# Optimization experiments

Hardware: AMD Instinct MI355X
Metric: run time of the kernel (lower is better)

## Reference

```python
import jax, jax.numpy as jnp
import numpy as np

BN_EPS = 1e-5


def _conv_bn_relu(x, w, gamma, beta):
    # 3x3 conv, stride 1, pad 1, no bias, NCHW; BatchNorm in training mode (batch stats)
    y = jax.lax.conv_general_dilated(x, w, (1, 1), ((1, 1), (1, 1)),
                                     dimension_numbers=('NCHW', 'OIHW', 'NCHW'))
    mu = y.mean(axis=(0, 2, 3), keepdims=True)
    var = y.var(axis=(0, 2, 3), keepdims=True)  # biased var, as torch BN uses for normalization
    y = (y - mu) * jax.lax.rsqrt(var + BN_EPS)
    y = y * gamma[None, :, None, None] + beta[None, :, None, None]
    return jax.nn.relu(y)


def setup_inputs() -> dict:
    key = jax.random.key(0)
    ks = jax.random.split(key, 12)
    N, C, h, w, H, W = 64, 256, 8, 8, 32, 32
    OC, NC = 256, 80
    inp = {
        'z_f': jax.random.normal(ks[0], (N, C, h, w), jnp.float32),
        'x_f': jax.random.normal(ks[1], (N, C, H, W), jnp.float32),
        'conv_cls_w': 0.05 * jax.random.normal(ks[2], (OC, C + 1, 3, 3), jnp.float32),
        'bn_cls_g': jnp.ones((OC,), jnp.float32),
        'bn_cls_b': jnp.zeros((OC,), jnp.float32),
        'conv_reg_w': 0.05 * jax.random.normal(ks[3], (OC, C + 1, 3, 3), jnp.float32),
        'bn_reg_g': jnp.ones((OC,), jnp.float32),
        'bn_reg_b': jnp.zeros((OC,), jnp.float32),
        'lin_cls_w': 0.01 * jax.random.normal(ks[4], (NC, OC * h * w), jnp.float32),
        'lin_cls_b': jnp.zeros((NC,), jnp.float32),
        'lin_reg_w': 0.01 * jax.random.normal(ks[5], (4 * NC, OC * H * W), jnp.float32),
        'lin_reg_b': jnp.zeros((4 * NC,), jnp.float32),
    }
    return inp


def reference(z_f, x_f, conv_cls_w, bn_cls_g, bn_cls_b, conv_reg_w, bn_reg_g, bn_reg_b,
              lin_cls_w, lin_cls_b, lin_reg_w, lin_reg_b):
    N, C, h, w = z_f.shape
    H, W = x_f.shape[2], x_f.shape[3]
    z = z_f.reshape(N, C, h * w)            # (N, C, hw)
    x = x_f.reshape(N, C, H * W)            # (N, C, HW)
    zt = z.transpose(0, 2, 1)               # (N, hw, C)
    xt = x.transpose(0, 2, 1)               # (N, HW, C)
    # batched pairwise squared-distance + sigmoid transform
    # NOTE: the original batched (ndim==3) path does NOT divide by sqrt(C)
    xs = jnp.sum(zt * zt, axis=-1)[:, :, None]          # (N, hw, 1)
    ys = jnp.sum(xt * xt, axis=-1)[:, None, :]          # (N, 1, HW)
    d = xs + ys - 2.0 * jnp.einsum('npc,nqc->npq', zt, xt)  # (N, hw, HW)
    d = 4.0 * jax.nn.sigmoid(-d) - 1.0     # == 4/(1+exp(d)) - 1, numerically stable
    dist_t = d.min(axis=1, keepdims=True)                    # (N, 1, HW)
    dist_s = d.min(axis=2, keepdims=True).transpose(0, 2, 1)  # (N, 1, hw)
    feat_cls = jnp.concatenate([dist_s, z], axis=1).reshape(N, C + 1, h, w)
    feat_loc = jnp.concatenate([dist_t, x], axis=1).reshape(N, C + 1, H, W)
    fc = _conv_bn_relu(feat_cls, conv_cls_w, bn_cls_g, bn_cls_b)   # (N, OC, h, w)
    fl = _conv_bn_relu(feat_loc, conv_reg_w, bn_reg_g, bn_reg_b)   # (N, OC, H, W)
    cls = fc.reshape(N, -1) @ lin_cls_w.T + lin_cls_b              # (N, n_classes)
    loc = fl.reshape(N, -1) @ lin_reg_w.T + lin_reg_b              # (N, 4*n_classes)
    return (cls, loc)
```

## Files before the change

kernel.cpp:

```cpp
#include <hip/hip_runtime.h>
#include <math.h>

typedef short short8 __attribute__((ext_vector_type(8)));
typedef float f32x4 __attribute__((ext_vector_type(4)));
typedef unsigned int uint4v __attribute__((ext_vector_type(4)));

#define WS_DS_ENC 0
#define WS_DT     4096
#define WS_SUMS   69632
#define WS_SS     70656
#define WS_YCLS   71680
#define WS_YREG   595968
#define WS_XT     8984576
#define WS_ZT     17373184
#define WS_WTR    17897472
#define WS_WTDR   18192384
#define WS_WTC    18196480
#define WS_WTDC   18491392
#define WS_PART   18495488
#define WS_XSQ    28981248
#define WS_ZSQ    29046784

__device__ __forceinline__ float dsig(float d) {
    return 4.0f / (1.0f + __expf(d)) - 1.0f;
}
__device__ __forceinline__ unsigned fenc(float f) {
    unsigned u = __float_as_uint(f);
    return (u & 0x80000000u) ? ~u : (u | 0x80000000u);
}
__device__ __forceinline__ float fdec(unsigned e) {
    unsigned u = (e & 0x80000000u) ? (e ^ 0x80000000u) : ~e;
    return __uint_as_float(u);
}
__device__ __forceinline__ unsigned short f2bf(float f) {
    unsigned u = __float_as_uint(f);
    return (unsigned short)((u + 0x7fffu + ((u >> 16) & 1u)) >> 16);
}
__device__ __forceinline__ float bf2f(unsigned short h) {
    return __uint_as_float(((unsigned)h) << 16);
}
__device__ __forceinline__ short8 pack8_trunc(const float* f) {
    uint4v u;
#pragma unroll
    for (int i = 0; i < 4; ++i) {
        unsigned lo = __float_as_uint(f[2 * i]) >> 16;
        unsigned hi = __float_as_uint(f[2 * i + 1]) & 0xffff0000u;
        u[i] = lo | hi;
    }
    return __builtin_bit_cast(short8, u);
}

__global__ void k_init(unsigned* __restrict__ ds_enc, float* __restrict__ sums,
                       float* __restrict__ out_cls, float* __restrict__ out_loc,
                       const float* __restrict__ lin_cls_b, const float* __restrict__ lin_reg_b) {
    int i = blockIdx.x * 256 + threadIdx.x;
    if (i < 4096) ds_enc[i] = 0u;
    if (i < 1024) sums[i] = 0.0f;
    if (i < 5120) out_cls[i] = lin_cls_b[i % 80];
    if (i < 20480) out_loc[i] = lin_reg_b[i % 320];
}

__global__ __launch_bounds__(256) void k_xt(const float* __restrict__ x, unsigned short* __restrict__ xt,
                                            float* __restrict__ xsq) {
    __shared__ float t[64 * 33];
    __shared__ float xr[4][32];
    const int n = blockIdx.x, row = blockIdx.y;
    const int tid = threadIdx.x;
    const int col = tid & 31, g = tid >> 5;
    float sq = 0.f;
    for (int c4 = 0; c4 < 4; ++c4) {
        const int ic0 = c4 * 64;
        __syncthreads();
        {
            int icl = tid >> 2, cg = tid & 3;
            const float* src = &x[((n * 256 + ic0 + icl) * 32 + row) * 32 + cg * 8];
            float4 a = *reinterpret_cast<const float4*>(src);
            float4 b = *reinterpret_cast<const float4*>(src + 4);
            float* d = &t[icl * 33 + cg * 8];
            d[0] = a.x; d[1] = a.y; d[2] = a.z; d[3] = a.w;
            d[4] = b.x; d[5] = b.y; d[6] = b.z; d[7] = b.w;
        }
        __syncthreads();
        {
            short8 v;
#pragma unroll
            for (int j = 0; j < 8; ++j) {
                float f = t[(g * 8 + j) * 33 + col];
                sq = fmaf(f, f, sq);
                v[j] = (short)f2bf(f);
            }
            *reinterpret_cast<short8*>(&xt[((n * 32 + row) * 32 + col) * 256 + ic0 + g * 8]) = v;
        }
    }
    sq += __shfl_xor(sq, 32);
    if ((tid & 63) < 32) xr[tid >> 6][col] = sq;
    __syncthreads();
    if (tid < 32) xsq[(n * 32 + row) * 32 + tid] = xr[0][tid] + xr[1][tid] + xr[2][tid] + xr[3][tid];
}

__global__ __launch_bounds__(256) void k_zt(const float* __restrict__ z, unsigned short* __restrict__ zt,
                                            float* __restrict__ zsq) {
    __shared__ float t[64 * 65];
    __shared__ float zr[4][64];
    const int n = blockIdx.x;
    const int tid = threadIdx.x;
    const int pos = tid & 63, gg = tid >> 6;
    float sq = 0.f;
    for (int c4 = 0; c4 < 4; ++c4) {
        const int ic0 = c4 * 64;
        __syncthreads();
        {
            int icl = tid >> 2, pg = tid & 3;
            const float* src = &z[(n * 256 + ic0 + icl) * 64 + pg * 16];
#pragma unroll
            for (int r = 0; r < 4; ++r) {
                float4 a = *reinterpret_cast<const float4*>(src + r * 4);
                float* d = &t[icl * 65 + pg * 16 + r * 4];
                d[0] = a.x; d[1] = a.y; d[2] = a.z; d[3] = a.w;
            }
        }
        __syncthreads();
        {
            short8 v0, v1;
#pragma unroll
            for (int j = 0; j < 8; ++j) {
                float f = t[(gg * 16 + j) * 65 + pos];
                sq = fmaf(f, f, sq);
                v0[j] = (short)f2bf(f);
            }
#pragma unroll
            for (int j = 0; j < 8; ++j) {
                float f = t[(gg * 16 + 8 + j) * 65 + pos];
                sq = fmaf(f, f, sq);
                v1[j] = (short)f2bf(f);
            }
            unsigned short* d = &zt[(n * 64 + pos) * 256 + ic0 + gg * 16];
            *reinterpret_cast<short8*>(d) = v0;
            *reinterpret_cast<short8*>(d + 8) = v1;
        }
    }
    zr[gg][pos] = sq;
    __syncthreads();
    if (tid < 64) zsq[n * 64 + tid] = zr[0][tid] + zr[1][tid] + zr[2][tid] + zr[3][tid];
}

__global__ void k_wswz(const float* __restrict__ wr, const float* __restrict__ wc,
                       unsigned short* __restrict__ wtr, unsigned short* __restrict__ wtdr,
                       unsigned short* __restrict__ wtc, unsigned short* __restrict__ wtdc) {
    const int idx = blockIdx.x * 256 + threadIdx.x;
    const float* src = blockIdx.y ? wc : wr;
    unsigned short* dw = blockIdx.y ? wtc : wtr;
    unsigned short* dd = blockIdx.y ? wtdc : wtdr;
    if (idx < 73728) {
        int tap = idx >> 13, rem = idx & 8191;
        int kc = rem >> 10, rem2 = rem & 1023;
        int q = rem2 >> 8, oc = rem2 & 255;
        short8 v;
#pragma unroll
        for (int j = 0; j < 8; ++j) {
            int icg = 1 + kc * 32 + q * 8 + j;
            v[j] = (short)f2bf(src[(oc * 257 + icg) * 9 + tap]);
        }
        *reinterpret_cast<short8*>(&dw[idx * 8]) = v;
    } else if (idx < 74752) {
        int i2 = idx - 73728;
        int q = i2 >> 8, oc = i2 & 255;
        short8 v;
#pragma unroll
        for (int j = 0; j < 8; ++j) {
            int k = q * 8 + j;
            v[j] = (k < 9) ? (short)f2bf(src[(oc * 257) * 9 + k]) : (short)0;
        }
        *reinterpret_cast<short8*>(&dd[i2 * 8]) = v;
    }
}

__global__ __launch_bounds__(256) void k_dist(const unsigned short* __restrict__ zt,
                                              const unsigned short* __restrict__ xt,
                                              const float* __restrict__ zsq, const float* __restrict__ xsq,
                                              float* __restrict__ dist_t, unsigned* __restrict__ ds_enc) {
    const int n = blockIdx.y;
    const int tid = threadIdx.x;
    const int wv = tid >> 6, lane = tid & 63;
    const int l15 = lane & 15, q4 = lane >> 4;
    const int q0 = blockIdx.x * 256 + wv * 64;
    const unsigned short* zb = zt + n * 16384;
    const unsigned short* xb = xt + (size_t)(n * 1024 + q0) * 256;

    f32x4 acc[4][4];
#pragma unroll
    for (int mi = 0; mi < 4; ++mi)
#pragma unroll
        for (int ni = 0; ni < 4; ++ni) acc[mi][ni] = (f32x4){0.f, 0.f, 0.f, 0.f};

#pragma unroll
    for (int ks = 0; ks < 8; ++ks) {
        short8 a[4], b[4];
#pragma unroll
        for (int mi = 0; mi < 4; ++mi)
            a[mi] = *reinterpret_cast<const short8*>(&zb[(mi * 16 + l15) * 256 + ks * 32 + q4 * 8]);
#pragma unroll
        for (int ni = 0; ni < 4; ++ni)
            b[ni] = *reinterpret_cast<const short8*>(&xb[(ni * 16 + l15) * 256 + ks * 32 + q4 * 8]);
#pragma unroll
        for (int ni = 0; ni < 4; ++ni)
#pragma unroll
            for (int mi = 0; mi < 4; ++mi)
                acc[mi][ni] = __builtin_amdgcn_mfma_f32_16x16x32_bf16(a[mi], b[ni], acc[mi][ni], 0, 0, 0);
    }

    float zs[4][4];
#pragma unroll
    for (int mi = 0; mi < 4; ++mi)
#pragma unroll
        for (int e = 0; e < 4; ++e) zs[mi][e] = zsq[n * 64 + mi * 16 + q4 * 4 + e];
    float xq[4];
#pragma unroll
    for (int ni = 0; ni < 4; ++ni) xq[ni] = xsq[n * 1024 + q0 + ni * 16 + l15];

#pragma unroll
    for (int ni = 0; ni < 4; ++ni) {
        float m = -1e30f;
#pragma unroll
        for (int mi = 0; mi < 4; ++mi)
#pragma unroll
            for (int e = 0; e < 4; ++e)
                m = fmaxf(m, zs[mi][e] - 2.f * acc[mi][ni][e]);
        m = fmaxf(m, __shfl_xor(m, 16));
        m = fmaxf(m, __shfl_xor(m, 32));
        if (lane < 16) dist_t[n * 1024 + q0 + ni * 16 + l15] = dsig(m + xq[ni]);
    }
#pragma unroll
    for (int mi = 0; mi < 4; ++mi)
#pragma unroll
        for (int e = 0; e < 4; ++e) {
            float v = -1e30f;
#pragma unroll
            for (int ni = 0; ni < 4; ++ni) v = fmaxf(v, xq[ni] - 2.f * acc[mi][ni][e]);
            v = fmaxf(v, __shfl_xor(v, 1));
            v = fmaxf(v, __shfl_xor(v, 2));
            v = fmaxf(v, __shfl_xor(v, 4));
            v = fmaxf(v, __shfl_xor(v, 8));
            if (l15 == 0) atomicMax(&ds_enc[n * 64 + mi * 16 + q4 * 4 + e], fenc(zs[mi][e] + v));
        }
}

__global__ __launch_bounds__(256) void k_conv_reg(
    const unsigned short* __restrict__ xt, const float* __restrict__ dist_t,
    const unsigned short* __restrict__ wt, const unsigned short* __restrict__ wtd,
    unsigned short* __restrict__ y, float* __restrict__ sums) {
    __shared__ __align__(16) char smem[17408];
    unsigned short* As = (unsigned short*)smem;
    unsigned short* Ds = (unsigned short*)(smem + 16320);
    float* Ts = (float*)smem;

    const int n = blockIdx.y;
    const int pt = blockIdx.x >> 1, ot = blockIdx.x & 1;
    const int tid = threadIdx.x;
    const int w = tid >> 6, lane = tid & 63;
    const int l15 = lane & 15, q = lane >> 4;
    const int wm = w & 1, wn = w >> 1;
    const int ocW = ot * 128 + wn * 64;

    f32x4 acc[4][4];
#pragma unroll
    for (int mi = 0; mi < 4; ++mi)
#pragma unroll
        for (int ni = 0; ni < 4; ++ni) acc[mi][ni] = (f32x4){0.f, 0.f, 0.f, 0.f};

    for (int f = tid; f < 204; f += 256) {
        int rr = f / 34, cc = f % 34;
        int prow = pt * 4 + rr;
        float v = 0.f;
        if (prow >= 1 && prow <= 32 && cc >= 1 && cc <= 32)
            v = dist_t[n * 1024 + (prow - 1) * 32 + (cc - 1)];
        Ds[f] = f2bf(v);
    }
    __syncthreads();
    {
        short8 ad[4];
#pragma unroll
        for (int mi = 0; mi < 4; ++mi) {
            int m = wm * 64 + mi * 16 + l15;
            int r = m >> 5, c = m & 31;
            short8 v = {0, 0, 0, 0, 0, 0, 0, 0};
#pragma unroll
            for (int j = 0; j < 8; ++j) {
                int k = q * 8 + j;
                if (k < 9) {
                    int ky = k / 3, kx = k % 3;
                    v[j] = (short)Ds[(r + ky) * 34 + (c + kx)];
                }
            }
            ad[mi] = v;
        }
#pragma unroll
        for (int ni = 0; ni < 4; ++ni) {
            short8 b = *reinterpret_cast<const short8*>(&wtd[(q * 256 + ocW + ni * 16 + l15) * 8]);
#pragma unroll
            for (int mi = 0; mi < 4; ++mi)
                acc[mi][ni] = __builtin_amdgcn_mfma_f32_16x16x32_bf16(ad[mi], b, acc[mi][ni], 0, 0, 0);
        }
    }

    for (int kc = 0; kc < 8; ++kc) {
        __syncthreads();
#pragma unroll
        for (int it = 0; it < 4; ++it) {
            int f = tid + 256 * it;
            if (f < 816) {
                int cell = f >> 2, ch = f & 3;
                int rr = cell / 34, cc = cell % 34;
                int prow = pt * 4 + rr;
                short8 v = {0, 0, 0, 0, 0, 0, 0, 0};
                if (prow >= 1 && prow <= 32 && cc >= 1 && cc <= 32)
                    v = *reinterpret_cast<const short8*>(
                        &xt[((n * 32 + prow - 1) * 32 + cc - 1) * 256 + kc * 32 + ch * 8]);
                *reinterpret_cast<short8*>(&As[cell * 40 + ch * 8]) = v;
            }
        }
        __syncthreads();
#pragma unroll
        for (int tap = 0; tap < 9; ++tap) {
            const int ky = tap / 3, kx = tap % 3;
            short8 a[4];
#pragma unroll
            for (int mi = 0; mi < 4; ++mi) {
                int m = wm * 64 + mi * 16 + l15;
                int r = (m >> 5) + ky, c = (m & 31) + kx;
                a[mi] = *reinterpret_cast<const short8*>(&As[(r * 34 + c) * 40 + q * 8]);
            }
            const unsigned short* wb = wt + (size_t)(((tap * 8 + kc) * 4 + q) * 256) * 8;
#pragma unroll
            for (int ni = 0; ni < 4; ++ni) {
                short8 b = *reinterpret_cast<const short8*>(&wb[(ocW + ni * 16 + l15) * 8]);
#pragma unroll
                for (int mi = 0; mi < 4; ++mi)
                    acc[mi][ni] = __builtin_amdgcn_mfma_f32_16x16x32_bf16(a[mi], b, acc[mi][ni], 0, 0, 0);
            }
        }
    }

#pragma unroll
    for (int ni = 0; ni < 4; ++ni) {
        float s = 0.f, qq = 0.f;
#pragma unroll
        for (int mi = 0; mi < 4; ++mi)
#pragma unroll
            for (int e = 0; e < 4; ++e) {
                float v = acc[mi][ni][e];
                s += v; qq = fmaf(v, v, qq);
            }
        s += __shfl_xor(s, 16); s += __shfl_xor(s, 32);
        qq += __shfl_xor(qq, 16); qq += __shfl_xor(qq, 32);
        if (lane < 16) {
            atomicAdd(&sums[512 + ocW + ni * 16 + l15], s);
            atomicAdd(&sums[768 + ocW + ni * 16 + l15], qq);
        }
    }

    __syncthreads();
    float* T = Ts + w * 1088;
#pragma unroll
    for (int mi = 0; mi < 4; ++mi) {
#pragma unroll
        for (int ni = 0; ni < 4; ++ni)
#pragma unroll
            for (int e = 0; e < 4; ++e)
                T[(ni * 16 + l15) * 17 + q * 4 + e] = acc[mi][ni][e];
#pragma unroll
        for (int eo = 0; eo < 16; ++eo) {
            int ocl = eo * 4 + q;
            float v = T[ocl * 17 + l15];
            y[(size_t)n * 262144 + (size_t)(ocW + ocl) * 1024 + pt * 128 + wm * 64 + mi * 16 + l15] = f2bf(v);
        }
    }
}

__global__ __launch_bounds__(256) void k_conv_cls(
    const unsigned short* __restrict__ zt, const unsigned* __restrict__ ds_enc,
    const unsigned short* __restrict__ wt, const unsigned short* __restrict__ wtd,
    unsigned short* __restrict__ y, float* __restrict__ sums) {
    __shared__ __align__(16) char smem[17408];
    unsigned short* As = (unsigned short*)smem;
    unsigned short* Ds = (unsigned short*)(smem + 16000);
    float* Ts = (float*)smem;

    const int n0 = blockIdx.x * 2;
    const int ob = blockIdx.y;
    const int tid = threadIdx.x;
    const int w = tid >> 6, lane = tid & 63;
    const int l15 = lane & 15, q = lane >> 4;
    const int wm = w & 1, wn = w >> 1;
    const int ocW = ob * 128 + wn * 64;

    f32x4 acc[4][4];
#pragma unroll
    for (int mi = 0; mi < 4; ++mi)
#pragma unroll
        for (int ni = 0; ni < 4; ++ni) acc[mi][ni] = (f32x4){0.f, 0.f, 0.f, 0.f};

    for (int f = tid; f < 200; f += 256) {
        int n_l = f / 100, rem = f % 100;
        int rr = rem / 10, cc = rem % 10;
        float v = 0.f;
        if (rr >= 1 && rr <= 8 && cc >= 1 && cc <= 8)
            v = dsig(fdec(ds_enc[(n0 + n_l) * 64 + (rr - 1) * 8 + (cc - 1)]));
        Ds[f] = f2bf(v);
    }
    __syncthreads();
    {
        short8 ad[4];
#pragma unroll
        for (int mi = 0; mi < 4; ++mi) {
            int pos = mi * 16 + l15;
            int r = pos >> 3, c = pos & 7;
            short8 v = {0, 0, 0, 0, 0, 0, 0, 0};
#pragma unroll
            for (int j = 0; j < 8; ++j) {
                int k = q * 8 + j;
                if (k < 9) {
                    int ky = k / 3, kx = k % 3;
                    v[j] = (short)Ds[wm * 100 + (r + ky) * 10 + (c + kx)];
                }
            }
            ad[mi] = v;
        }
#pragma unroll
        for (int ni = 0; ni < 4; ++ni) {
            short8 b = *reinterpret_cast<const short8*>(&wtd[(q * 256 + ocW + ni * 16 + l15) * 8]);
#pragma unroll
            for (int mi = 0; mi < 4; ++mi)
                acc[mi][ni] = __builtin_amdgcn_mfma_f32_16x16x32_bf16(ad[mi], b, acc[mi][ni], 0, 0, 0);
        }
    }

    for (int kc = 0; kc < 8; ++kc) {
        __syncthreads();
#pragma unroll
        for (int it = 0; it < 4; ++it) {
            int f = tid + 256 * it;
            if (f < 800) {
                int cell = f >> 2, ch = f & 3;
                int n_l = cell / 100, rem = cell % 100;
                int rr = rem / 10, cc = rem % 10;
                short8 v = {0, 0, 0, 0, 0, 0, 0, 0};
                if (rr >= 1 && rr <= 8 && cc >= 1 && cc <= 8)
                    v = *reinterpret_cast<const short8*>(
                        &zt[((n0 + n_l) * 64 + (rr - 1) * 8 + (cc - 1)) * 256 + kc * 32 + ch * 8]);
                *reinterpret_cast<short8*>(&As[cell * 40 + ch * 8]) = v;
            }
        }
        __syncthreads();
#pragma unroll
        for (int tap = 0; tap < 9; ++tap) {
            const int ky = tap / 3, kx = tap % 3;
            short8 a[4];
#pragma unroll
            for (int mi = 0; mi < 4; ++mi) {
                int pos = mi * 16 + l15;
                int r = (pos >> 3) + ky, c = (pos & 7) + kx;
                a[mi] = *reinterpret_cast<const short8*>(&As[(wm * 100 + r * 10 + c) * 40 + q * 8]);
            }
            const unsigned short* wb = wt + (size_t)(((tap * 8 + kc) * 4 + q) * 256) * 8;
#pragma unroll
            for (int ni = 0; ni < 4; ++ni) {
                short8 b = *reinterpret_cast<const short8*>(&wb[(ocW + ni * 16 + l15) * 8]);
#pragma unroll
                for (int mi = 0; mi < 4; ++mi)
                    acc[mi][ni] = __builtin_amdgcn_mfma_f32_16x16x32_bf16(a[mi], b, acc[mi][ni], 0, 0, 0);
            }
        }
    }

#pragma unroll
    for (int ni = 0; ni < 4; ++ni) {
        float s = 0.f, qq = 0.f;
#pragma unroll
        for (int mi = 0; mi < 4; ++mi)
#pragma unroll
            for (int e = 0; e < 4; ++e) {
                float v = acc[mi][ni][e];
                s += v; qq = fmaf(v, v, qq);
            }
        s += __shfl_xor(s, 16); s += __shfl_xor(s, 32);
        qq += __shfl_xor(qq, 16); qq += __shfl_xor(qq, 32);
        if (lane < 16) {
            atomicAdd(&sums[0 + ocW + ni * 16 + l15], s);
            atomicAdd(&sums[256 + ocW + ni * 16 + l15], qq);
        }
    }

    __syncthreads();
    float* T = Ts + w * 1088;
#pragma unroll
    for (int mi = 0; mi < 4; ++mi) {
#pragma unroll
        for (int ni = 0; ni < 4; ++ni)
#pragma unroll
            for (int e = 0; e < 4; ++e)
                T[(ni * 16 + l15) * 17 + q * 4 + e] = acc[mi][ni][e];
#pragma unroll
        for (int eo = 0; eo < 16; ++eo) {
            int ocl = eo * 4 + q;
            float v = T[ocl * 17 + l15];
            y[(size_t)(n0 + wm) * 16384 + (size_t)(ocW + ocl) * 64 + mi * 16 + l15] = f2bf(v);
        }
    }
}

__global__ void k_bnfin(const float* __restrict__ sums,
                        const float* __restrict__ g_cls, const float* __restrict__ b_cls,
                        const float* __restrict__ g_reg, const float* __restrict__ b_reg,
                        float* __restrict__ ss) {
    int t = threadIdx.x;
    {
        float mean = sums[t] * (1.f / 4096.f);
        float var = sums[256 + t] * (1.f / 4096.f) - mean * mean;
        float sc = g_cls[t] * rsqrtf(var + 1e-5f);
        ss[t] = sc;
        ss[256 + t] = b_cls[t] - mean * sc;
    }
    {
        float mean = sums[512 + t] * (1.f / 65536.f);
        float var = sums[768 + t] * (1.f / 65536.f) - mean * mean;
        float sc = g_reg[t] * rsqrtf(var + 1e-5f);
        ss[512 + t] = sc;
        ss[768 + t] = b_reg[t] - mean * sc;
    }
}

__global__ __launch_bounds__(256) void k_lin_cls(const unsigned short* __restrict__ y, const float* __restrict__ ss,
                                                 const float* __restrict__ w, float* __restrict__ out) {
    const int kb = blockIdx.x * 256;
    const int tid = threadIdx.x;
    const int wv = tid >> 6, lane = tid & 63;
    const int l15 = lane & 15, q4 = lane >> 4;
    f32x4 acc[5];
#pragma unroll
    for (int ni = 0; ni < 5; ++ni) acc[ni] = (f32x4){0.f, 0.f, 0.f, 0.f};
#pragma unroll
    for (int ks = 0; ks < 8; ++ks) {
        const int k0 = kb + ks * 32 + q4 * 8;
        short8 yv = *reinterpret_cast<const short8*>(&y[(wv * 16 + l15) * 16384 + k0]);
        const int ch = k0 >> 6;
        const float sc = ss[ch], sh = ss[256 + ch];
        float f[8];
#pragma unroll
        for (int j = 0; j < 8; ++j) f[j] = fmaxf(fmaf(bf2f((unsigned short)yv[j]), sc, sh), 0.f);
        short8 a = pack8_trunc(f);
#pragma unroll
        for (int ni = 0; ni < 5; ++ni) {
            const float* wp = &w[(size_t)(ni * 16 + l15) * 16384 + k0];
            float4 b0 = *reinterpret_cast<const float4*>(wp);
            float4 b1 = *reinterpret_cast<const float4*>(wp + 4);
            float g[8] = {b0.x, b0.y, b0.z, b0.w, b1.x, b1.y, b1.z, b1.w};
            acc[ni] = __builtin_amdgcn_mfma_f32_16x16x32_bf16(a, pack8_trunc(g), acc[ni], 0, 0, 0);
        }
    }
#pragma unroll
    for (int ni = 0; ni < 5; ++ni)
#pragma unroll
        for (int e = 0; e < 4; ++e)
            atomicAdd(&out[(wv * 16 + q4 * 4 + e) * 80 + ni * 16 + l15], acc[ni][e]);
}

__global__ __launch_bounds__(256) void k_lin_reg2(const unsigned short* __restrict__ y, const float* __restrict__ ss,
                                                  const float* __restrict__ w, float* __restrict__ part) {
    __shared__ __align__(16) unsigned short A_l[32 * 520];
    const int k0 = blockIdx.x * 512;
    const int tid = threadIdx.x;
    const int wv = tid >> 6, lane = tid & 63;
    const int l15 = lane & 15, q = lane >> 4;
    const int jw = wv * 80;

    f32x4 acc[5][4];
#pragma unroll
    for (int ni = 0; ni < 5; ++ni)
#pragma unroll
        for (int mi = 0; mi < 4; ++mi) acc[ni][mi] = (f32x4){0.f, 0.f, 0.f, 0.f};

    for (int scn = 0; scn < 2; ++scn) {
        const int ksub = k0 + scn * 256;
        const int ch = ksub >> 10;
        const float scf = ss[512 + ch], shf = ss[768 + ch];
        __syncthreads();
        {
            const int c = tid & 31, nb = tid >> 5;
#pragma unroll
            for (int p = 0; p < 8; ++p) {
                const int n = p * 8 + nb;
                short8 v = *reinterpret_cast<const short8*>(&y[(size_t)n * 262144 + ksub + c * 8]);
                float f[8];
#pragma unroll
                for (int j = 0; j < 8; ++j)
                    f[j] = fmaxf(fmaf(bf2f((unsigned short)v[j]), scf, shf), 0.f);
                *reinterpret_cast<short8*>(&A_l[c * 520 + n * 8]) = pack8_trunc(f);
            }
        }
        __syncthreads();
#pragma unroll
        for (int kk = 0; kk < 8; ++kk) {
            short8 a[4];
#pragma unroll
            for (int mi = 0; mi < 4; ++mi)
                a[mi] = *reinterpret_cast<const short8*>(&A_l[(kk * 4 + q) * 520 + (mi * 16 + l15) * 8]);
            short8 b[5];
#pragma unroll
            for (int ni = 0; ni < 5; ++ni) {
                const float* wp = &w[(size_t)(jw + ni * 16 + l15) * 262144 + ksub + kk * 32 + q * 8];
                float4 b0 = *reinterpret_cast<const float4*>(wp);
                float4 b1 = *reinterpret_cast<const float4*>(wp + 4);
                float f[8] = {b0.x, b0.y, b0.z, b0.w, b1.x, b1.y, b1.z, b1.w};
                b[ni] = pack8_trunc(f);
            }
#pragma unroll
            for (int ni = 0; ni < 5; ++ni)
#pragma unroll
                for (int mi = 0; mi < 4; ++mi)
                    acc[ni][mi] = __builtin_amdgcn_mfma_f32_16x16x32_bf16(a[mi], b[ni], acc[ni][mi], 0, 0, 0);
        }
    }

    float* pb = part + (size_t)blockIdx.x * 20480;
#pragma unroll
    for (int ni = 0; ni < 5; ++ni) {
        const int j = jw + ni * 16 + l15;
#pragma unroll
        for (int mi = 0; mi < 4; ++mi)
#pragma unroll
            for (int e = 0; e < 4; ++e) {
                const int n = mi * 16 + q * 4 + e;
                pb[n * 320 + j] = acc[ni][mi][e];
            }
    }
}

__global__ __launch_bounds__(256) void k_lin_red(const float* __restrict__ part, float* __restrict__ out_loc) {
    const int idx = blockIdx.x * 256 + threadIdx.x;
    const int b0 = blockIdx.y * 128;
    float s0 = 0.f, s1 = 0.f, s2 = 0.f, s3 = 0.f;
#pragma unroll 4
    for (int b = 0; b < 128; b += 4) {
        s0 += part[(size_t)(b0 + b + 0) * 20480 + idx];
        s1 += part[(size_t)(b0 + b + 1) * 20480 + idx];
        s2 += part[(size_t)(b0 + b + 2) * 20480 + idx];
        s3 += part[(size_t)(b0 + b + 3) * 20480 + idx];
    }
    atomicAdd(&out_loc[idx], (s0 + s1) + (s2 + s3));
}

extern "C" void kernel_launch(void* const* d_in, const int* in_sizes, int n_in,
                              void* d_out, int out_size, void* d_ws, size_t ws_size,
                              hipStream_t stream) {
    const float* z_f        = (const float*)d_in[0];
    const float* x_f        = (const float*)d_in[1];
    const float* conv_cls_w = (const float*)d_in[2];
    const float* bn_cls_g   = (const float*)d_in[3];
    const float* bn_cls_b   = (const float*)d_in[4];
    const float* conv_reg_w = (const float*)d_in[5];
    const float* bn_reg_g   = (const float*)d_in[6];
    const float* bn_reg_b   = (const float*)d_in[7];
    const float* lin_cls_w  = (const float*)d_in[8];
    const float* lin_cls_b  = (const float*)d_in[9];
    const float* lin_reg_w  = (const float*)d_in[10];
    const float* lin_reg_b  = (const float*)d_in[11];

    float* out = (float*)d_out;
    float* ws  = (float*)d_ws;
    unsigned* ds_enc = (unsigned*)(ws + WS_DS_ENC);
    float* dist_t = ws + WS_DT;
    float* sums   = ws + WS_SUMS;
    float* ss     = ws + WS_SS;
    unsigned short* y_cls = (unsigned short*)(ws + WS_YCLS);
    unsigned short* y_reg = (unsigned short*)(ws + WS_YREG);
    unsigned short* xt    = (unsigned short*)(ws + WS_XT);
    unsigned short* zt    = (unsigned short*)(ws + WS_ZT);
    unsigned short* wtr   = (unsigned short*)(ws + WS_WTR);
    unsigned short* wtdr  = (unsigned short*)(ws + WS_WTDR);
    unsigned short* wtc   = (unsigned short*)(ws + WS_WTC);
    unsigned short* wtdc  = (unsigned short*)(ws + WS_WTDC);
    float* part   = ws + WS_PART;
    float* xsq    = ws + WS_XSQ;
    float* zsq    = ws + WS_ZSQ;

    hipLaunchKernelGGL(k_init, dim3(80), dim3(256), 0, stream, ds_enc, sums, out, out + 5120, lin_cls_b, lin_reg_b);
    hipLaunchKernelGGL(k_xt, dim3(64, 32), dim3(256), 0, stream, x_f, xt, xsq);
    hipLaunchKernelGGL(k_zt, dim3(64), dim3(256), 0, stream, z_f, zt, zsq);
    hipLaunchKernelGGL(k_wswz, dim3(292, 2), dim3(256), 0, stream, conv_reg_w, conv_cls_w, wtr, wtdr, wtc, wtdc);
    hipLaunchKernelGGL(k_dist, dim3(4, 64), dim3(256), 0, stream, zt, xt, zsq, xsq, dist_t, ds_enc);
    hipLaunchKernelGGL(k_conv_reg, dim3(16, 64), dim3(256), 0, stream, xt, dist_t, wtr, wtdr, y_reg, sums);
    hipLaunchKernelGGL(k_conv_cls, dim3(32, 2), dim3(256), 0, stream, zt, ds_enc, wtc, wtdc, y_cls, sums);
    hipLaunchKernelGGL(k_bnfin, dim3(1), dim3(256), 0, stream, sums, bn_cls_g, bn_cls_b, bn_reg_g, bn_reg_b, ss);
    hipLaunchKernelGGL(k_lin_cls, dim3(64), dim3(256), 0, stream, y_cls, ss, lin_cls_w, out);
    hipLaunchKernelGGL(k_lin_reg2, dim3(512), dim3(256), 0, stream, y_reg, ss, lin_reg_w, part);
    hipLaunchKernelGGL(k_lin_red, dim3(80, 4), dim3(256), 0, stream, part, out + 5120);
}
```

Before: 791.7 us.

## Merge prep, conv, and linear kernels into fewer launches with double-buffered conv staging

New measurement: 761.5 us. -3.8%, faster.

```diff
diff --git a/kernel.cpp b/kernel.cpp
--- a/kernel.cpp
+++ b/kernel.cpp
@@ -49,129 +49,136 @@
     }
     return __builtin_bit_cast(short8, u);
 }
-
-__global__ void k_init(unsigned* __restrict__ ds_enc, float* __restrict__ sums,
-                       float* __restrict__ out_cls, float* __restrict__ out_loc,
-                       const float* __restrict__ lin_cls_b, const float* __restrict__ lin_reg_b) {
-    int i = blockIdx.x * 256 + threadIdx.x;
-    if (i < 4096) ds_enc[i] = 0u;
-    if (i < 1024) sums[i] = 0.0f;
-    if (i < 5120) out_cls[i] = lin_cls_b[i % 80];
-    if (i < 20480) out_loc[i] = lin_reg_b[i % 320];
-}
-
-__global__ __launch_bounds__(256) void k_xt(const float* __restrict__ x, unsigned short* __restrict__ xt,
-                                            float* __restrict__ xsq) {
-    __shared__ float t[64 * 33];
-    __shared__ float xr[4][32];
-    const int n = blockIdx.x, row = blockIdx.y;
+__device__ __forceinline__ void barrier_lgkm() {
+    asm volatile("s_waitcnt lgkmcnt(0)" ::: "memory");
+    __builtin_amdgcn_s_barrier();
+    __builtin_amdgcn_sched_barrier(0);
+}
+
+__global__ __launch_bounds__(256) void k_prep(
+    const float* __restrict__ x, const float* __restrict__ z,
+    const float* __restrict__ wr, const float* __restrict__ wc,
+    unsigned short* __restrict__ xt, unsigned short* __restrict__ zt,
+    float* __restrict__ xsq, float* __restrict__ zsq,
+    unsigned short* __restrict__ wtr, unsigned short* __restrict__ wtdr,
+    unsigned short* __restrict__ wtc, unsigned short* __restrict__ wtdc,
+    unsigned* __restrict__ ds_enc, float* __restrict__ sums,
+    float* __restrict__ out_cls, float* __restrict__ out_loc,
+    const float* __restrict__ lin_cls_b, const float* __restrict__ lin_reg_b) {
+    __shared__ __align__(16) char pmem[17920];
+    const int b = blockIdx.x;
     const int tid = threadIdx.x;
-    const int col = tid & 31, g = tid >> 5;
-    float sq = 0.f;
-    for (int c4 = 0; c4 < 4; ++c4) {
-        const int ic0 = c4 * 64;
+    if (b < 2048) {
+        float* t = (float*)pmem;
+        float* xr = (float*)(pmem + 8448);
+        const int n = b >> 5, row = b & 31;
+        const int col = tid & 31, g = tid >> 5;
+        float sq = 0.f;
+        for (int c4 = 0; c4 < 4; ++c4) {
+            const int ic0 = c4 * 64;
+            __syncthreads();
+            {
+                int icl = tid >> 2, cg = tid & 3;
+                const float* src = &x[((n * 256 + ic0 + icl) * 32 + row) * 32 + cg * 8];
+                float4 a = *reinterpret_cast<const float4*>(src);
+                float4 bb = *reinterpret_cast<const float4*>(src + 4);
+                float* d = &t[icl * 33 + cg * 8];
+                d[0] = a.x; d[1] = a.y; d[2] = a.z; d[3] = a.w;
+                d[4] = bb.x; d[5] = bb.y; d[6] = bb.z; d[7] = bb.w;
+            }
+            __syncthreads();
+            {
+                short8 v;
+#pragma unroll
+                for (int j = 0; j < 8; ++j) {
+                    float f = t[(g * 8 + j) * 33 + col];
+                    sq = fmaf(f, f, sq);
+                    v[j] = (short)f2bf(f);
+                }
+                *reinterpret_cast<short8*>(&xt[((n * 32 + row) * 32 + col) * 256 + ic0 + g * 8]) = v;
+            }
+        }
+        sq += __shfl_xor(sq, 32);
+        if ((tid & 63) < 32) xr[(tid >> 6) * 32 + col] = sq;
         __syncthreads();
-        {
-            int icl = tid >> 2, cg = tid & 3;
-            const float* src = &x[((n * 256 + ic0 + icl) * 32 + row) * 32 + cg * 8];
-            float4 a = *reinterpret_cast<const float4*>(src);
-            float4 b = *reinterpret_cast<const float4*>(src + 4);
-            float* d = &t[icl * 33 + cg * 8];
-            d[0] = a.x; d[1] = a.y; d[2] = a.z; d[3] = a.w;
-            d[4] = b.x; d[5] = b.y; d[6] = b.z; d[7] = b.w;
-        }
+        if (tid < 32) xsq[(n * 32 + row) * 32 + tid] = xr[tid] + xr[32 + tid] + xr[64 + tid] + xr[96 + tid];
+    } else if (b < 2112) {
+        float* t = (float*)pmem;
+        float* zr = (float*)(pmem + 16640);
+        const int n = b - 2048;
+        const int pos = tid & 63, gg = tid >> 6;
+        float sq = 0.f;
+        for (int c4 = 0; c4 < 4; ++c4) {
+            const int ic0 = c4 * 64;
+            __syncthreads();
+            {
+                int icl = tid >> 2, pg = tid & 3;
+                const float* src = &z[(n * 256 + ic0 + icl) * 64 + pg * 16];
+#pragma unroll
+                for (int r = 0; r < 4; ++r) {
+                    float4 a = *reinterpret_cast<const float4*>(src + r * 4);
+                    float* d = &t[icl * 65 + pg * 16 + r * 4];
+                    d[0] = a.x; d[1] = a.y; d[2] = a.z; d[3] = a.w;
+                }
+            }
+            __syncthreads();
+            {
+                short8 v0, v1;
+#pragma unroll
+                for (int j = 0; j < 8; ++j) {
+                    float f = t[(gg * 16 + j) * 65 + pos];
+                    sq = fmaf(f, f, sq);
+                    v0[j] = (short)f2bf(f);
+                }
+#pragma unroll
+                for (int j = 0; j < 8; ++j) {
+                    float f = t[(gg * 16 + 8 + j) * 65 + pos];
+                    sq = fmaf(f, f, sq);
+                    v1[j] = (short)f2bf(f);
+                }
+                unsigned short* d = &zt[(n * 64 + pos) * 256 + ic0 + gg * 16];
+                *reinterpret_cast<short8*>(d) = v0;
+                *reinterpret_cast<short8*>(d + 8) = v1;
+            }
+        }
+        zr[gg * 64 + pos] = sq;
         __syncthreads();
-        {
+        if (tid < 64) zsq[n * 64 + tid] = zr[tid] + zr[64 + tid] + zr[128 + tid] + zr[192 + tid];
+    } else if (b < 2696) {
+        const int sub = b - 2112;
+        const int by = sub / 292, bx = sub % 292;
+        const int idx = bx * 256 + tid;
+        const float* src = by ? wc : wr;
+        unsigned short* dw = by ? wtc : wtr;
+        unsigned short* dd = by ? wtdc : wtdr;
+        if (idx < 73728) {
+            int tap = idx >> 13, rem = idx & 8191;
+            int kc = rem >> 10, rem2 = rem & 1023;
+            int q = rem2 >> 8, oc = rem2 & 255;
             short8 v;
 #pragma unroll
             for (int j = 0; j < 8; ++j) {
-                float f = t[(g * 8 + j) * 33 + col];
-                sq = fmaf(f, f, sq);
-                v[j] = (short)f2bf(f);
-            }
-            *reinterpret_cast<short8*>(&xt[((n * 32 + row) * 32 + col) * 256 + ic0 + g * 8]) = v;
-        }
-    }
-    sq += __shfl_xor(sq, 32);
-    if ((tid & 63) < 32) xr[tid >> 6][col] = sq;
-    __syncthreads();
-    if (tid < 32) xsq[(n * 32 + row) * 32 + tid] = xr[0][tid] + xr[1][tid] + xr[2][tid] + xr[3][tid];
-}
-
-__global__ __launch_bounds__(256) void k_zt(const float* __restrict__ z, unsigned short* __restrict__ zt,
-                                            float* __restrict__ zsq) {
-    __shared__ float t[64 * 65];
-    __shared__ float zr[4][64];
-    const int n = blockIdx.x;
-    const int tid = threadIdx.x;
-    const int pos = tid & 63, gg = tid >> 6;
-    float sq = 0.f;
-    for (int c4 = 0; c4 < 4; ++c4) {
-        const int ic0 = c4 * 64;
-        __syncthreads();
-        {
-            int icl = tid >> 2, pg = tid & 3;
-            const float* src = &z[(n * 256 + ic0 + icl) * 64 + pg * 16];
-#pragma unroll
-            for (int r = 0; r < 4; ++r) {
-                float4 a = *reinterpret_cast<const float4*>(src + r * 4);
-                float* d = &t[icl * 65 + pg * 16 + r * 4];
-                d[0] = a.x; d[1] = a.y; d[2] = a.z; d[3] = a.w;
-            }
-        }
-        __syncthreads();
-        {
-            short8 v0, v1;
+                int icg = 1 + kc * 32 + q * 8 + j;
+                v[j] = (short)f2bf(src[(oc * 257 + icg) * 9 + tap]);
+            }
+            *reinterpret_cast<short8*>(&dw[idx * 8]) = v;
+        } else if (idx < 74752) {
+            int i2 = idx - 73728;
+            int q = i2 >> 8, oc = i2 & 255;
+            short8 v;
 #pragma unroll
             for (int j = 0; j < 8; ++j) {
-                float f = t[(gg * 16 + j) * 65 + pos];
-                sq = fmaf(f, f, sq);
-                v0[j] = (short)f2bf(f);
-            }
-#pragma unroll
-            for (int j = 0; j < 8; ++j) {
-                float f = t[(gg * 16 + 8 + j) * 65 + pos];
-                sq = fmaf(f, f, sq);
-                v1[j] = (short)f2bf(f);
-            }
-            unsigned short* d = &zt[(n * 64 + pos) * 256 + ic0 + gg * 16];
-            *reinterpret_cast<short8*>(d) = v0;
-            *reinterpret_cast<short8*>(d + 8) = v1;
-        }
-    }
-    zr[gg][pos] = sq;
-    __syncthreads();
-    if (tid < 64) zsq[n * 64 + tid] = zr[0][tid] + zr[1][tid] + zr[2][tid] + zr[3][tid];
-}
-
-__global__ void k_wswz(const float* __restrict__ wr, const float* __restrict__ wc,
-                       unsigned short* __restrict__ wtr, unsigned short* __restrict__ wtdr,
-                       unsigned short* __restrict__ wtc, unsigned short* __restrict__ wtdc) {
-    const int idx = blockIdx.x * 256 + threadIdx.x;
-    const float* src = blockIdx.y ? wc : wr;
-    unsigned short* dw = blockIdx.y ? wtc : wtr;
-    unsigned short* dd = blockIdx.y ? wtdc : wtdr;
-    if (idx < 73728) {
-        int tap = idx >> 13, rem = idx & 8191;
-        int kc = rem >> 10, rem2 = rem & 1023;
-        int q = rem2 >> 8, oc = rem2 & 255;
-        short8 v;
-#pragma unroll
-        for (int j = 0; j < 8; ++j) {
-            int icg = 1 + kc * 32 + q * 8 + j;
-            v[j] = (short)f2bf(src[(oc * 257 + icg) * 9 + tap]);
-        }
-        *reinterpret_cast<short8*>(&dw[idx * 8]) = v;
-    } else if (idx < 74752) {
-        int i2 = idx - 73728;
-        int q = i2 >> 8, oc = i2 & 255;
-        short8 v;
-#pragma unroll
-        for (int j = 0; j < 8; ++j) {
-            int k = q * 8 + j;
-            v[j] = (k < 9) ? (short)f2bf(src[(oc * 257) * 9 + k]) : (short)0;
-        }
-        *reinterpret_cast<short8*>(&dd[i2 * 8]) = v;
+                int k = q * 8 + j;
+                v[j] = (k < 9) ? (short)f2bf(src[(oc * 257) * 9 + k]) : (short)0;
+            }
+            *reinterpret_cast<short8*>(&dd[i2 * 8]) = v;
+        }
+    } else {
+        const int i = (b - 2696) * 256 + tid;
+        if (i < 4096) ds_enc[i] = 0u;
+        if (i < 1024) sums[i] = 0.0f;
+        if (i < 5120) out_cls[i] = lin_cls_b[i % 80];
+        if (i < 20480) out_loc[i] = lin_reg_b[i % 320];
     }
 }
 
@@ -245,22 +252,23 @@
         }
 }
 
-__global__ __launch_bounds__(256) void k_conv_reg(
+__global__ __launch_bounds__(256) void k_conv(
     const unsigned short* __restrict__ xt, const float* __restrict__ dist_t,
-    const unsigned short* __restrict__ wt, const unsigned short* __restrict__ wtd,
-    unsigned short* __restrict__ y, float* __restrict__ sums) {
-    __shared__ __align__(16) char smem[17408];
-    unsigned short* As = (unsigned short*)smem;
-    unsigned short* Ds = (unsigned short*)(smem + 16320);
+    const unsigned short* __restrict__ zt, const unsigned* __restrict__ ds_enc,
+    const unsigned short* __restrict__ wtr, const unsigned short* __restrict__ wtdr,
+    const unsigned short* __restrict__ wtc, const unsigned short* __restrict__ wtdc,
+    unsigned short* __restrict__ y_reg, unsigned short* __restrict__ y_cls,
+    float* __restrict__ sums) {
+    __shared__ __align__(16) char smem[33056];
+    unsigned short* As0 = (unsigned short*)smem;
+    unsigned short* As1 = (unsigned short*)(smem + 16320);
+    unsigned short* Ds = (unsigned short*)(smem + 32640);
     float* Ts = (float*)smem;
 
-    const int n = blockIdx.y;
-    const int pt = blockIdx.x >> 1, ot = blockIdx.x & 1;
     const int tid = threadIdx.x;
     const int w = tid >> 6, lane = tid & 63;
     const int l15 = lane & 15, q = lane >> 4;
     const int wm = w & 1, wn = w >> 1;
-    const int ocW = ot * 128 + wn * 64;
 
     f32x4 acc[4][4];
 #pragma unroll
@@ -268,380 +276,412 @@
 #pragma unroll
         for (int ni = 0; ni < 4; ++ni) acc[mi][ni] = (f32x4){0.f, 0.f, 0.f, 0.f};
 
-    for (int f = tid; f < 204; f += 256) {
-        int rr = f / 34, cc = f % 34;
-        int prow = pt * 4 + rr;
-        float v = 0.f;
-        if (prow >= 1 && prow <= 32 && cc >= 1 && cc <= 32)
-            v = dist_t[n * 1024 + (prow - 1) * 32 + (cc - 1)];
-        Ds[f] = f2bf(v);
-    }
-    __syncthreads();
-    {
-        short8 ad[4];
-#pragma unroll
-        for (int mi = 0; mi < 4; ++mi) {
-            int m = wm * 64 + mi * 16 + l15;
-            int r = m >> 5, c = m & 31;
-            short8 v = {0, 0, 0, 0, 0, 0, 0, 0};
-#pragma unroll
-            for (int j = 0; j < 8; ++j) {
-                int k = q * 8 + j;
-                if (k < 9) {
-                    int ky = k / 3, kx = k % 3;
-                    v[j] = (short)Ds[(r + ky) * 34 + (c + kx)];
-                }
-            }
-            ad[mi] = v;
-        }
-#pragma unroll
-        for (int ni = 0; ni < 4; ++ni) {
-            short8 b = *reinterpret_cast<const short8*>(&wtd[(q * 256 + ocW + ni * 16 + l15) * 8]);
-#pragma unroll
-            for (int mi = 0; mi < 4; ++mi)
-                acc[mi][ni] = __builtin_amdgcn_mfma_f32_16x16x32_bf16(ad[mi], b, acc[mi][ni], 0, 0, 0);
-        }
-    }
-
-    for (int kc = 0; kc < 8; ++kc) {
+    if (blockIdx.x < 1024) {
+        const int n = blockIdx.x >> 4, bx = blockIdx.x & 15;
+        const int pt = bx >> 1, ot = bx & 1;
+        const int ocW = ot * 128 + wn * 64;
+
+        for (int f = tid; f < 204; f += 256) {
+            int rr = f / 34, cc = f % 34;
+            int prow = pt * 4 + rr;
+            float v = 0.f;
+            if (prow >= 1 && prow <= 32 && cc >= 1 && cc <= 32)
+                v = dist_t[n * 1024 + (prow - 1) * 32 + (cc - 1)];
+            Ds[f] = f2bf(v);
+        }
         __syncthreads();
+        {
+            short8 ad[4];
+#pragma unroll
+            for (int mi = 0; mi < 4; ++mi) {
+                int m = wm * 64 + mi * 16 + l15;
+                int r = m >> 5, c = m & 31;
+                short8 v = {0, 0, 0, 0, 0, 0, 0, 0};
+#pragma unroll
+                for (int j = 0; j < 8; ++j) {
+                    int k = q * 8 + j;
+                    if (k < 9) {
+                        int ky = k / 3, kx = k % 3;
+                        v[j] = (short)Ds[(r + ky) * 34 + (c + kx)];
+                    }
+                }
+                ad[mi] = v;
+            }
+#pragma unroll
+            for (int ni = 0; ni < 4; ++ni) {
+                short8 bfr = *reinterpret_cast<const short8*>(&wtdr[(q * 256 + ocW + ni * 16 + l15) * 8]);
+#pragma unroll
+                for (int mi = 0; mi < 4; ++mi)
+                    acc[mi][ni] = __builtin_amdgcn_mfma_f32_16x16x32_bf16(ad[mi], bfr, acc[mi][ni], 0, 0, 0);
+            }
+        }
+
+        int ldso[4]; size_t go[4]; bool gv[4], wvld[4];
 #pragma unroll
         for (int it = 0; it < 4; ++it) {
             int f = tid + 256 * it;
-            if (f < 816) {
-                int cell = f >> 2, ch = f & 3;
-                int rr = cell / 34, cc = cell % 34;
-                int prow = pt * 4 + rr;
+            int cell = f >> 2, chn = f & 3;
+            int rr = cell / 34, cc = cell % 34;
+            int prow = pt * 4 + rr;
+            wvld[it] = (f < 816);
+            gv[it] = wvld[it] && prow >= 1 && prow <= 32 && cc >= 1 && cc <= 32;
+            go[it] = ((size_t)(n * 32 + prow - 1) * 32 + (cc - 1)) * 256 + chn * 8;
+            ldso[it] = cell * 40 + chn * 8;
+        }
+        short8 st[4];
+#pragma unroll
+        for (int it = 0; it < 4; ++it) {
+            short8 v = {0, 0, 0, 0, 0, 0, 0, 0};
+            if (gv[it]) v = *reinterpret_cast<const short8*>(&xt[go[it]]);
+            st[it] = v;
+        }
+        for (int kc = 0; kc < 8; ++kc) {
+            unsigned short* As = (kc & 1) ? As1 : As0;
+#pragma unroll
+            for (int it = 0; it < 4; ++it)
+                if (wvld[it]) *reinterpret_cast<short8*>(&As[ldso[it]]) = st[it];
+            if (kc < 7) {
+#pragma unroll
+                for (int it = 0; it < 4; ++it) {
+                    short8 v = {0, 0, 0, 0, 0, 0, 0, 0};
+                    if (gv[it]) v = *reinterpret_cast<const short8*>(&xt[go[it] + (kc + 1) * 32]);
+                    st[it] = v;
+                }
+            }
+            barrier_lgkm();
+#pragma unroll
+            for (int tap = 0; tap < 9; ++tap) {
+                const int ky = tap / 3, kx = tap % 3;
+                short8 a[4];
+#pragma unroll
+                for (int mi = 0; mi < 4; ++mi) {
+                    int m = wm * 64 + mi * 16 + l15;
+                    int r = (m >> 5) + ky, c = (m & 31) + kx;
+                    a[mi] = *reinterpret_cast<const short8*>(&As[(r * 34 + c) * 40 + q * 8]);
+                }
+                const unsigned short* wb = wtr + (size_t)(((tap * 8 + kc) * 4 + q) * 256) * 8;
+#pragma unroll
+                for (int ni = 0; ni < 4; ++ni) {
+                    short8 bfr = *reinterpret_cast<const short8*>(&wb[(ocW + ni * 16 + l15) * 8]);
+#pragma unroll
+                    for (int mi = 0; mi < 4; ++mi)
+                        acc[mi][ni] = __builtin_amdgcn_mfma_f32_16x16x32_bf16(a[mi], bfr, acc[mi][ni], 0, 0, 0);
+                }
+            }
+        }
+
+#pragma unroll
+        for (int ni = 0; ni < 4; ++ni) {
+            float s = 0.f, qq = 0.f;
+#pragma unroll
+            for (int mi = 0; mi < 4; ++mi)
+#pragma unroll
+                for (int e = 0; e < 4; ++e) {
+                    float v = acc[mi][ni][e];
+                    s += v; qq = fmaf(v, v, qq);
+                }
+            s += __shfl_xor(s, 16); s += __shfl_xor(s, 32);
+            qq += __shfl_xor(qq, 16); qq += __shfl_xor(qq, 32);
+            if (lane < 16) {
+                atomicAdd(&sums[512 + ocW + ni * 16 + l15], s);
+                atomicAdd(&sums[768 + ocW + ni * 16 + l15], qq);
+            }
+        }
+
+        __syncthreads();
+        float* T = Ts + w * 1088;
+#pragma unroll
+        for (int mi = 0; mi < 4; ++mi) {
+#pragma unroll
+            for (int ni = 0; ni < 4; ++ni)
+#pragma unroll
+                for (int e = 0; e < 4; ++e)
+                    T[(ni * 16 + l15) * 17 + q * 4 + e] = acc[mi][ni][e];
+#pragma unroll
+            for (int eo = 0; eo < 16; ++eo) {
+                int ocl = eo * 4 + q;
+                float v = T[ocl * 17 + l15];
+                y_reg[(size_t)n * 262144 + (size_t)(ocW + ocl) * 1024 + pt * 128 + wm * 64 + mi * 16 + l15] = f2bf(v);
+            }
+        }
+    } else {
+        const int sub = blockIdx.x - 1024;
+        const int n0 = (sub & 31) * 2;
+        const int ob = sub >> 5;
+        const int ocW = ob * 128 + wn * 64;
+
+        for (int f = tid; f < 200; f += 256) {
+            int n_l = f / 100, rem = f % 100;
+            int rr = rem / 10, cc = rem % 10;
+            float v = 0.f;
+            if (rr >= 1 && rr <= 8 && cc >= 1 && cc <= 8)
+                v = dsig(fdec(ds_enc[(n0 + n_l) * 64 + (rr - 1) * 8 + (cc - 1)]));
+            Ds[f] = f2bf(v);
+        }
+        __syncthreads();
+        {
+            short8 ad[4];
+#pragma unroll
+            for (int mi = 0; mi < 4; ++mi) {
+                int pos = mi * 16 + l15;
+                int r = pos >> 3, c = pos & 7;
                 short8 v = {0, 0, 0, 0, 0, 0, 0, 0};
-                if (prow >= 1 && prow <= 32 && cc >= 1 && cc <= 32)
-                    v = *reinterpret_cast<const short8*>(
-                        &xt[((n * 32 + prow - 1) * 32 + cc - 1) * 256 + kc * 32 + ch * 8]);
-                *reinterpret_cast<short8*>(&As[cell * 40 + ch * 8]) = v;
-            }
-        }
-        __syncthreads();
-#pragma unroll
-        for (int tap = 0; tap < 9; ++tap) {
-            const int ky = tap / 3, kx = tap % 3;
-            short8 a[4];
-#pragma unroll
-            for (int mi = 0; mi < 4; ++mi) {
-                int m = wm * 64 + mi * 16 + l15;
-                int r = (m >> 5) + ky, c = (m & 31) + kx;
-                a[mi] = *reinterpret_cast<const short8*>(&As[(r * 34 + c) * 40 + q * 8]);
-            }
-            const unsigned short* wb = wt + (size_t)(((tap * 8 + kc) * 4 + q) * 256) * 8;
+#pragma unroll
+                for (int j = 0; j < 8; ++j) {
+                    int k = q * 8 + j;
+                    if (k < 9) {
+                        int ky = k / 3, kx = k % 3;
+                        v[j] = (short)Ds[wm * 100 + (r + ky) * 10 + (c + kx)];
+                    }
+                }
+                ad[mi] = v;
+            }
 #pragma unroll
             for (int ni = 0; ni < 4; ++ni) {
-                short8 b = *reinterpret_cast<const short8*>(&wb[(ocW + ni * 16 + l15) * 8]);
+                short8 bfr = *reinterpret_cast<const short8*>(&wtdc[(q * 256 + ocW + ni * 16 + l15) * 8]);
 #pragma unroll
                 for (int mi = 0; mi < 4; ++mi)
-                    acc[mi][ni] = __builtin_amdgcn_mfma_f32_16x16x32_bf16(a[mi], b, acc[mi][ni], 0, 0, 0);
-            }
-        }
-    }
-
-#pragma unroll
-    for (int ni = 0; ni < 4; ++ni) {
-        float s = 0.f, qq = 0.f;
-#pragma unroll
-        for (int mi = 0; mi < 4; ++mi)
-#pragma unroll
-            for (int e = 0; e < 4; ++e) {
-                float v = acc[mi][ni][e];
-                s += v; qq = fmaf(v, v, qq);
-            }
-        s += __shfl_xor(s, 16); s += __shfl_xor(s, 32);
-        qq += __shfl_xor(qq, 16); qq += __shfl_xor(qq, 32);
-        if (lane < 16) {
-            atomicAdd(&sums[512 + ocW + ni * 16 + l15], s);
-            atomicAdd(&sums[768 + ocW + ni * 16 + l15], qq);
-        }
-    }
-
-    __syncthreads();
-    float* T = Ts + w * 1088;
-#pragma unroll
-    for (int mi = 0; mi < 4; ++mi) {
-#pragma unroll
-        for (int ni = 0; ni < 4; ++ni)
-#pragma unroll
-            for (int e = 0; e < 4; ++e)
-                T[(ni * 16 + l15) * 17 + q * 4 + e] = acc[mi][ni][e];
-#pragma unroll
-        for (int eo = 0; eo < 16; ++eo) {
-            int ocl = eo * 4 + q;
-            float v = T[ocl * 17 + l15];
-            y[(size_t)n * 262144 + (size_t)(ocW + ocl) * 1024 + pt * 128 + wm * 64 + mi * 16 + l15] = f2bf(v);
-        }
-    }
-}
-
-__global__ __launch_bounds__(256) void k_conv_cls(
-    const unsigned short* __restrict__ zt, const unsigned* __restrict__ ds_enc,
-    const unsigned short* __restrict__ wt, const unsigned short* __restrict__ wtd,
-    unsigned short* __restrict__ y, float* __restrict__ sums) {
-    __shared__ __align__(16) char smem[17408];
-    unsigned short* As = (unsigned short*)smem;
-    unsigned short* Ds = (unsigned short*)(smem + 16000);
-    float* Ts = (float*)smem;
-
-    const int n0 = blockIdx.x * 2;
-    const int ob = blockIdx.y;
-    const int tid = threadIdx.x;
-    const int w = tid >> 6, lane = tid & 63;
-    const int l15 = lane & 15, q = lane >> 4;
-    const int wm = w & 1, wn = w >> 1;
-    const int ocW = ob * 128 + wn * 64;
-
-    f32x4 acc[4][4];
-#pragma unroll
-    for (int mi = 0; mi < 4; ++mi)
-#pragma unroll
-        for (int ni = 0; ni < 4; ++ni) acc[mi][ni] = (f32x4){0.f, 0.f, 0.f, 0.f};
-
-    for (int f = tid; f < 200; f += 256) {
-        int n_l = f / 100, rem = f % 100;
-        int rr = rem / 10, cc = rem % 10;
-        float v = 0.f;
-        if (rr >= 1 && rr <= 8 && cc >= 1 && cc <= 8)
-            v = dsig(fdec(ds_enc[(n0 + n_l) * 64 + (rr - 1) * 8 + (cc - 1)]));
-        Ds[f] = f2bf(v);
-    }
-    __syncthreads();
-    {
-        short8 ad[4];
-#pragma unroll
-        for (int mi = 0; mi < 4; ++mi) {
-            int pos = mi * 16 + l15;
-            int r = pos >> 3, c = pos & 7;
-            short8 v = {0, 0, 0, 0, 0, 0, 0, 0};
-#pragma unroll
-            for (int j = 0; j < 8; ++j) {
-                int k = q * 8 + j;
-                if (k < 9) {
-                    int ky = k / 3, kx = k % 3;
-                    v[j] = (short)Ds[wm * 100 + (r + ky) * 10 + (c + kx)];
-                }
-            }
-            ad[mi] = v;
-        }
-#pragma unroll
-        for (int ni = 0; ni < 4; ++ni) {
-            short8 b = *reinterpret_cast<const short8*>(&wtd[(q * 256 + ocW + ni * 16 + l15) * 8]);
-#pragma unroll
-            for (int mi = 0; mi < 4; ++mi)
-                acc[mi][ni] = __builtin_amdgcn_mfma_f32_16x16x32_bf16(ad[mi], b, acc[mi][ni], 0, 0, 0);
-        }
-    }
-
-    for (int kc = 0; kc < 8; ++kc) {
-        __syncthreads();
+                    acc[mi][ni] = __builtin_amdgcn_mfma_f32_16x16x32_bf16(ad[mi], bfr, acc[mi][ni], 0, 0, 0);
+            }
+        }
+
+        int ldso[4]; size_t go[4]; bool gv[4], wvld[4];
 #pragma unroll
         for (int it = 0; it < 4; ++it) {
             int f = tid + 256 * it;
-            if (f < 800) {
-                int cell = f >> 2, ch = f & 3;
-                int n_l = cell / 100, rem = cell % 100;
-                int rr = rem / 10, cc = rem % 10;
-                short8 v = {0, 0, 0, 0, 0, 0, 0, 0};
-                if (rr >= 1 && rr <= 8 && cc >= 1 && cc <= 8)
-                    v = *reinterpret_cast<const short8*>(
-                        &zt[((n0 + n_l) * 64 + (rr - 1) * 8 + (cc - 1)) * 256 + kc * 32 + ch * 8]);
-                *reinterpret_cast<short8*>(&As[cell * 40 + ch * 8]) = v;
-            }
-        }
+            int cell = f >> 2, chn = f & 3;
+            int n_l = cell / 100, rem = cell % 100;
+            int rr = rem / 10, cc = rem % 10;
+            wvld[it] = (f < 800);
+            gv[it] = wvld[it] && rr >= 1 && rr <= 8 && cc >= 1 && cc <= 8;
+            go[it] = ((size_t)((n0 + n_l) * 64 + (rr - 1) * 8 + (cc - 1))) * 256 + chn * 8;
+            ldso[it] = cell * 40 + chn * 8;
+        }
+        short8 st[4];
+#pragma unroll
+        for (int it = 0; it < 4; ++it) {
+            short8 v = {0, 0, 0, 0, 0, 0, 0, 0};
+            if (gv[it]) v = *reinterpret_cast<const short8*>(&zt[go[it]]);
+            st[it] = v;
+        }
+        for (int kc = 0; kc < 8; ++kc) {
+            unsigned short* As = (kc & 1) ? As1 : As0;
+#pragma unroll
+            for (int it = 0; it < 4; ++it)
+                if (wvld[it]) *reinterpret_cast<short8*>(&As[ldso[it]]) = st[it];
+            if (kc < 7) {
+#pragma unroll
+                for (int it = 0; it < 4; ++it) {
+                    short8 v = {0, 0, 0, 0, 0, 0, 0, 0};
+                    if (gv[it]) v = *reinterpret_cast<const short8*>(&zt[go[it] + (kc + 1) * 32]);
+                    st[it] = v;
+                }
+            }
+            barrier_lgkm();
+#pragma unroll
+            for (int tap = 0; tap < 9; ++tap) {
+                const int ky = tap / 3, kx = tap % 3;
+                short8 a[4];
+#pragma unroll
+                for (int mi = 0; mi < 4; ++mi) {
+                    int pos = mi * 16 + l15;
+                    int r = (pos >> 3) + ky, c = (pos & 7) + kx;
+                    a[mi] = *reinterpret_cast<const short8*>(&As[(wm * 100 + r * 10 + c) * 40 + q * 8]);
+                }
+                const unsigned short* wb = wtc + (size_t)(((tap * 8 + kc) * 4 + q) * 256) * 8;
+#pragma unroll
+                for (int ni = 0; ni < 4; ++ni) {
+                    short8 bfr = *reinterpret_cast<const short8*>(&wb[(ocW + ni * 16 + l15) * 8]);
+#pragma unroll
+                    for (int mi = 0; mi < 4; ++mi)
+                        acc[mi][ni] = __builtin_amdgcn_mfma_f32_16x16x32_bf16(a[mi], bfr, acc[mi][ni], 0, 0, 0);
+                }
+            }
+        }
+
+#pragma unroll
+        for (int ni = 0; ni < 4; ++ni) {
+            float s = 0.f, qq = 0.f;
+#pragma unroll
+            for (int mi = 0; mi < 4; ++mi)
+#pragma unroll
+                for (int e = 0; e < 4; ++e) {
+                    float v = acc[mi][ni][e];
+                    s += v; qq = fmaf(v, v, qq);
+                }
+            s += __shfl_xor(s, 16); s += __shfl_xor(s, 32);
+            qq += __shfl_xor(qq, 16); qq += __shfl_xor(qq, 32);
+            if (lane < 16) {
+                atomicAdd(&sums[0 + ocW + ni * 16 + l15], s);
+                atomicAdd(&sums[256 + ocW + ni * 16 + l15], qq);
+            }
+        }
+
         __syncthreads();
-#pragma unroll
-        for (int tap = 0; tap < 9; ++tap) {
-            const int ky = tap / 3, kx = tap % 3;
-            short8 a[4];
-#pragma unroll
-            for (int mi = 0; mi < 4; ++mi) {
-                int pos = mi * 16 + l15;
-                int r = (pos >> 3) + ky, c = (pos & 7) + kx;
-                a[mi] = *reinterpret_cast<const short8*>(&As[(wm * 100 + r * 10 + c) * 40 + q * 8]);
-            }
-            const unsigned short* wb = wt + (size_t)(((tap * 8 + kc) * 4 + q) * 256) * 8;
-#pragma unroll
-            for (int ni = 0; ni < 4; ++ni) {
-                short8 b = *reinterpret_cast<const short8*>(&wb[(ocW + ni * 16 + l15) * 8]);
-#pragma unroll
-                for (int mi = 0; mi < 4; ++mi)
-                    acc[mi][ni] = __builtin_amdgcn_mfma_f32_16x16x32_bf16(a[mi], b, acc[mi][ni], 0, 0, 0);
+        float* T = Ts + w * 1088;
+#pragma unroll
+        for (int mi = 0; mi < 4; ++mi) {
+#pragma unroll
+            for (int ni = 0; ni < 4; ++ni)
+#pragma unroll
+                for (int e = 0; e < 4; ++e)
+                    T[(ni * 16 + l15) * 17 + q * 4 + e] = acc[mi][ni][e];
+#pragma unroll
+            for (int eo = 0; eo < 16; ++eo) {
+                int ocl = eo * 4 + q;
+                float v = T[ocl * 17 + l15];
+                y_cls[(size_t)(n0 + wm) * 16384 + (size_t)(ocW + ocl) * 64 + mi * 16 + l15] = f2bf(v);
             }
         }
     }
-
-#pragma unroll
-    for (int ni = 0; ni < 4; ++ni) {
-        float s = 0.f, qq = 0.f;
-#pragma unroll
-        for (int mi = 0; mi < 4; ++mi)
-#pragma unroll
-            for (int e = 0; e < 4; ++e) {
-                float v = acc[mi][ni][e];
-                s += v; qq = fmaf(v, v, qq);
-            }
-        s += __shfl_xor(s, 16); s += __shfl_xor(s, 32);
-        qq += __shfl_xor(qq, 16); qq += __shfl_xor(qq, 32);
-        if (lane < 16) {
-            atomicAdd(&sums[0 + ocW + ni * 16 + l15], s);
-            atomicAdd(&sums[256 + ocW + ni * 16 + l15], qq);
-        }
-    }
-
-    __syncthreads();
-    float* T = Ts + w * 1088;
-#pragma unroll
-    for (int mi = 0; mi < 4; ++mi) {
-#pragma unroll
-        for (int ni = 0; ni < 4; ++ni)
-#pragma unroll
-            for (int e = 0; e < 4; ++e)
-                T[(ni * 16 + l15) * 17 + q * 4 + e] = acc[mi][ni][e];
-#pragma unroll
-        for (int eo = 0; eo < 16; ++eo) {
-            int ocl = eo * 4 + q;
-            float v = T[ocl * 17 + l15];
-            y[(size_t)(n0 + wm) * 16384 + (size_t)(ocW + ocl) * 64 + mi * 16 + l15] = f2bf(v);
-        }
-    }
-}
-
-__global__ void k_bnfin(const float* __restrict__ sums,
-                        const float* __restrict__ g_cls, const float* __restrict__ b_cls,
-                        const float* __restrict__ g_reg, const float* __restrict__ b_reg,
-                        float* __restrict__ ss) {
-    int t = threadIdx.x;
-    {
-        float mean = sums[t] * (1.f / 4096.f);
-        float var = sums[256 + t] * (1.f / 4096.f) - mean * mean;
-        float sc = g_cls[t] * rsqrtf(var + 1e-5f);
-        ss[t] = sc;
-        ss[256 + t] = b_cls[t] - mean * sc;
-    }
-    {
-        float mean = sums[512 + t] * (1.f / 65536.f);
-        float var = sums[768 + t] * (1.f / 65536.f) - mean * mean;
-        float sc = g_reg[t] * rsqrtf(var + 1e-5f);
-        ss[512 + t] = sc;
-        ss[768 + t] = b_reg[t] - mean * sc;
-    }
-}
-
-__global__ __launch_bounds__(256) void k_lin_cls(const unsigned short* __restrict__ y, const float* __restrict__ ss,
-                                                 const float* __restrict__ w, float* __restrict__ out) {
-    const int kb = blockIdx.x * 256;
-    const int tid = threadIdx.x;
-    const int wv = tid >> 6, lane = tid & 63;
-    const int l15 = lane & 15, q4 = lane >> 4;
-    f32x4 acc[5];
-#pragma unroll
-    for (int ni = 0; ni < 5; ++ni) acc[ni] = (f32x4){0.f, 0.f, 0.f, 0.f};
-#pragma unroll
-    for (int ks = 0; ks < 8; ++ks) {
-        const int k0 = kb + ks * 32 + q4 * 8;
-        short8 yv = *reinterpret_cast<const short8*>(&y[(wv * 16 + l15) * 16384 + k0]);
-        const int ch = k0 >> 6;
-        const float sc = ss[ch], sh = ss[256 + ch];
-        float f[8];
-#pragma unroll
-        for (int j = 0; j < 8; ++j) f[j] = fmaxf(fmaf(bf2f((unsigned short)yv[j]), sc, sh), 0.f);
-        short8 a = pack8_trunc(f);
-#pragma unroll
-        for (int ni = 0; ni < 5; ++ni) {
-            const float* wp = &w[(size_t)(ni * 16 + l15) * 16384 + k0];
-            float4 b0 = *reinterpret_cast<const float4*>(wp);
-            float4 b1 = *reinterpret_cast<const float4*>(wp + 4);
-            float g[8] = {b0.x, b0.y, b0.z, b0.w, b1.x, b1.y, b1.z, b1.w};
-            acc[ni] = __builtin_amdgcn_mfma_f32_16x16x32_bf16(a, pack8_trunc(g), acc[ni], 0, 0, 0);
-        }
-    }
-#pragma unroll
-    for (int ni = 0; ni < 5; ++ni)
-#pragma unroll
-        for (int e = 0; e < 4; ++e)
-            atomicAdd(&out[(wv * 16 + q4 * 4 + e) * 80 + ni * 16 + l15], acc[ni][e]);
-}
-
-__global__ __launch_bounds__(256) void k_lin_reg2(const unsigned short* __restrict__ y, const float* __restrict__ ss,
-                                                  const float* __restrict__ w, float* __restrict__ part) {
-    __shared__ __align__(16) unsigned short A_l[32 * 520];
-    const int k0 = blockIdx.x * 512;
+}
+
+__global__ __launch_bounds__(256) void k_lin(
+    const unsigned short* __restrict__ y_reg, const unsigned short* __restrict__ y_cls,
+    const float* __restrict__ sums,
+    const float* __restrict__ g_cls, const float* __restrict__ b_cls,
+    const float* __restrict__ g_reg, const float* __restrict__ b_reg,
+    const float* __restrict__ w_reg, const float* __restrict__ w_cls,
+    float* __restrict__ part, float* __restrict__ out_cls) {
+    __shared__ __align__(16) char smem[35328];
     const int tid = threadIdx.x;
     const int wv = tid >> 6, lane = tid & 63;
     const int l15 = lane & 15, q = lane >> 4;
-    const int jw = wv * 80;
-
-    f32x4 acc[5][4];
-#pragma unroll
-    for (int ni = 0; ni < 5; ++ni)
-#pragma unroll
-        for (int mi = 0; mi < 4; ++mi) acc[ni][mi] = (f32x4){0.f, 0.f, 0.f, 0.f};
-
-    for (int scn = 0; scn < 2; ++scn) {
-        const int ksub = k0 + scn * 256;
-        const int ch = ksub >> 10;
-        const float scf = ss[512 + ch], shf = ss[768 + ch];
+
+    if (blockIdx.x < 512) {
+        unsigned short* A_l = (unsigned short*)smem;
+        float* ss_l = (float*)(smem + 33280);
+        {
+            float mean = sums[512 + tid] * (1.f / 65536.f);
+            float var = sums[768 + tid] * (1.f / 65536.f) - mean * mean;
+            float sc = g_reg[tid] * rsqrtf(var + 1e-5f);
+            ss_l[tid] = sc;
+            ss_l[256 + tid] = b_reg[tid] - mean * sc;
+        }
+        const int k0 = blockIdx.x * 512;
+        const int jw = wv * 80;
+
+        f32x4 acc[5][4];
+#pragma unroll
+        for (int ni = 0; ni < 5; ++ni)
+#pragma unroll
+            for (int mi = 0; mi < 4; ++mi) acc[ni][mi] = (f32x4){0.f, 0.f, 0.f, 0.f};
+
+        for (int scn = 0; scn < 2; ++scn) {
+            const int ksub = k0 + scn * 256;
+            const int ch = ksub >> 10;
+            __syncthreads();
+            const float scf = ss_l[ch], shf = ss_l[256 + ch];
+            {
+                const int c = tid & 31, nb = tid >> 5;
+#pragma unroll
+                for (int p = 0; p < 8; ++p) {
+                    const int n = p * 8 + nb;
+                    short8 v = *reinterpret_cast<const short8*>(&y_reg[(size_t)n * 262144 + ksub + c * 8]);
+                    float f[8];
+#pragma unroll
+                    for (int j = 0; j < 8; ++j)
+                        f[j] = fmaxf(fmaf(bf2f((unsigned short)v[j]), scf, shf), 0.f);
+                    *reinterpret_cast<short8*>(&A_l[c * 520 + n * 8]) = pack8_trunc(f);
+                }
+            }
+            __syncthreads();
+            float4 w0[5], w1[5];
+#pragma unroll
+            for (int ni = 0; ni < 5; ++ni) {
+                const float* wp = &w_reg[(size_t)(jw + ni * 16 + l15) * 262144 + ksub + q * 8];
+                w0[ni] = *reinterpret_cast<const float4*>(wp);
+                w1[ni] = *reinterpret_cast<const float4*>(wp + 4);
+            }
+#pragma unroll
+            for (int kk = 0; kk < 8; ++kk) {
+                short8 b[5];
+#pragma unroll
+                for (int ni = 0; ni < 5; ++ni) {
+                    float f[8] = {w0[ni].x, w0[ni].y, w0[ni].z, w0[ni].w,
+                                  w1[ni].x, w1[ni].y, w1[ni].z, w1[ni].w};
+                    b[ni] = pack8_trunc(f);
+                }
+                if (kk < 7) {
+#pragma unroll
+                    for (int ni = 0; ni < 5; ++ni) {
+                        const float* wp = &w_reg[(size_t)(jw + ni * 16 + l15) * 262144 + ksub + (kk + 1) * 32 + q * 8];
+                        w0[ni] = *reinterpret_cast<const float4*>(wp);
+                        w1[ni] = *reinterpret_cast<const float4*>(wp + 4);
+                    }
+                }
+                short8 a[4];
+#pragma unroll
+                for (int mi = 0; mi < 4; ++mi)
+                    a[mi] = *reinterpret_cast<const short8*>(&A_l[(kk * 4 + q) * 520 + (mi * 16 + l15) * 8]);
+#pragma unroll
+                for (int ni = 0; ni < 5; ++ni)
+#pragma unroll
+                    for (int mi = 0; mi < 4; ++mi)
+                        acc[ni][mi] = __builtin_amdgcn_mfma_f32_16x16x32_bf16(a[mi], b[ni], acc[ni][mi], 0, 0, 0);
+            }
+        }
+
+        float* pb = part + (size_t)blockIdx.x * 20480;
+#pragma unroll
+        for (int ni = 0; ni < 5; ++ni) {
+            const int j = jw + ni * 16 + l15;
+#pragma unroll
+            for (int mi = 0; mi < 4; ++mi)
+#pragma unroll
+                for (int e = 0; e < 4; ++e) {
+                    const int n = mi * 16 + q * 4 + e;
+                    pb[n * 320 + j] = acc[ni][mi][e];
+                }
+        }
+    } else {
+        float* ss_l = (float*)smem;
+        {
+            float mean = sums[tid] * (1.f / 4096.f);
+            float var = sums[256 + tid] * (1.f / 4096.f) - mean * mean;
+            float sc = g_cls[tid] * rsqrtf(var + 1e-5f);
+            ss_l[tid] = sc;
+            ss_l[256 + tid] = b_cls[tid] - mean * sc;
+        }
         __syncthreads();
-        {
-            const int c = tid & 31, nb = tid >> 5;
-#pragma unroll
-            for (int p = 0; p < 8; ++p) {
-                const int n = p * 8 + nb;
-                short8 v = *reinterpret_cast<const short8*>(&y[(size_t)n * 262144 + ksub + c * 8]);
-                float f[8];
-#pragma unroll
-                for (int j = 0; j < 8; ++j)
-                    f[j] = fmaxf(fmaf(bf2f((unsigned short)v[j]), scf, shf), 0.f);
-                *reinterpret_cast<short8*>(&A_l[c * 520 + n * 8]) = pack8_trunc(f);
-            }
-        }
-        __syncthreads();
-#pragma unroll
-        for (int kk = 0; kk < 8; ++kk) {
-            short8 a[4];
-#pragma unroll
-            for (int mi = 0; mi < 4; ++mi)
-                a[mi] = *reinterpret_cast<const short8*>(&A_l[(kk * 4 + q) * 520 + (mi * 16 + l15) * 8]);
-            short8 b[5];
+        const int kb = (blockIdx.x - 512) * 256;
+        const int q4 = q;
+        f32x4 acc[5];
+#pragma unroll
+        for (int ni = 0; ni < 5; ++ni) acc[ni] = (f32x4){0.f, 0.f, 0.f, 0.f};
+#pragma unroll
+        for (int ks = 0; ks < 8; ++ks) {
+            const int kx = kb + ks * 32 + q4 * 8;
+            short8 yv = *reinterpret_cast<const short8*>(&y_cls[(wv * 16 + l15) * 16384 + kx]);
+            const int ch = kx >> 6;
+            const float sc = ss_l[ch], sh = ss_l[256 + ch];
+            float f[8];
+#pragma unroll
+            for (int j = 0; j < 8; ++j) f[j] = fmaxf(fmaf(bf2f((unsigned short)yv[j]), sc, sh), 0.f);
+            short8 a = pack8_trunc(f);
 #pragma unroll
             for (int ni = 0; ni < 5; ++ni) {
-                const float* wp = &w[(size_t)(jw + ni * 16 + l15) * 262144 + ksub + kk * 32 + q * 8];
+                const float* wp = &w_cls[(size_t)(ni * 16 + l15) * 16384 + kx];
                 float4 b0 = *reinterpret_cast<const float4*>(wp);
                 float4 b1 = *reinterpret_cast<const float4*>(wp + 4);
-                float f[8] = {b0.x, b0.y, b0.z, b0.w, b1.x, b1.y, b1.z, b1.w};
-                b[ni] = pack8_trunc(f);
-            }
-#pragma unroll
-            for (int ni = 0; ni < 5; ++ni)
-#pragma unroll
-                for (int mi = 0; mi < 4; ++mi)
-                    acc[ni][mi] = __builtin_amdgcn_mfma_f32_16x16x32_bf16(a[mi], b[ni], acc[ni][mi], 0, 0, 0);
-        }
-    }
-
-    float* pb = part + (size_t)blockIdx.x * 20480;
-#pragma unroll
-    for (int ni = 0; ni < 5; ++ni) {
-        const int j = jw + ni * 16 + l15;
-#pragma unroll
-        for (int mi = 0; mi < 4; ++mi)
-#pragma unroll
-            for (int e = 0; e < 4; ++e) {
-                const int n = mi * 16 + q * 4 + e;
-                pb[n * 320 + j] = acc[ni][mi][e];
-            }
+                float g[8] = {b0.x, b0.y, b0.z, b0.w, b1.x, b1.y, b1.z, b1.w};
+                acc[ni] = __builtin_amdgcn_mfma_f32_16x16x32_bf16(a, pack8_trunc(g), acc[ni], 0, 0, 0);
+            }
+        }
+#pragma unroll
+        for (int ni = 0; ni < 5; ++ni)
+#pragma unroll
+            for (int e = 0; e < 4; ++e)
+                atomicAdd(&out_cls[(wv * 16 + q4 * 4 + e) * 80 + ni * 16 + l15], acc[ni][e]);
     }
 }
 
 __global__ __launch_bounds__(256) void k_lin_red(const float* __restrict__ part, float* __restrict__ out_loc) {
     const int idx = blockIdx.x * 256 + threadIdx.x;
-    const int b0 = blockIdx.y * 128;
+    const int b0 = blockIdx.y * 64;
     float s0 = 0.f, s1 = 0.f, s2 = 0.f, s3 = 0.f;
 #pragma unroll 4
-    for (int b = 0; b < 128; b += 4) {
+    for (int b = 0; b < 64; b += 4) {
         s0 += part[(size_t)(b0 + b + 0) * 20480 + idx];
         s1 += part[(size_t)(b0 + b + 1) * 20480 + idx];
         s2 += part[(size_t)(b0 + b + 2) * 20480 + idx];
@@ -671,7 +711,6 @@
     unsigned* ds_enc = (unsigned*)(ws + WS_DS_ENC);
     float* dist_t = ws + WS_DT;
     float* sums   = ws + WS_SUMS;
-    float* ss     = ws + WS_SS;
     unsigned short* y_cls = (unsigned short*)(ws + WS_YCLS);
     unsigned short* y_reg = (unsigned short*)(ws + WS_YREG);
     unsigned short* xt    = (unsigned short*)(ws + WS_XT);
@@ -684,15 +723,14 @@
     float* xsq    = ws + WS_XSQ;
     float* zsq    = ws + WS_ZSQ;
 
-    hipLaunchKernelGGL(k_init, dim3(80), dim3(256), 0, stream, ds_enc, sums, out, out + 5120, lin_cls_b, lin_reg_b);
-    hipLaunchKernelGGL(k_xt, dim3(64, 32), dim3(256), 0, stream, x_f, xt, xsq);
-    hipLaunchKernelGGL(k_zt, dim3(64), dim3(256), 0, stream, z_f, zt, zsq);
-    hipLaunchKernelGGL(k_wswz, dim3(292, 2), dim3(256), 0, stream, conv_reg_w, conv_cls_w, wtr, wtdr, wtc, wtdc);
+    hipLaunchKernelGGL(k_prep, dim3(2776), dim3(256), 0, stream,
+                       x_f, z_f, conv_reg_w, conv_cls_w, xt, zt, xsq, zsq,
+                       wtr, wtdr, wtc, wtdc, ds_enc, sums, out, out + 5120, lin_cls_b, lin_reg_b);
     hipLaunchKernelGGL(k_dist, dim3(4, 64), dim3(256), 0, stream, zt, xt, zsq, xsq, dist_t, ds_enc);
-    hipLaunchKernelGGL(k_conv_reg, dim3(16, 64), dim3(256), 0, stream, xt, dist_t, wtr, wtdr, y_reg, sums);
-    hipLaunchKernelGGL(k_conv_cls, dim3(32, 2), dim3(256), 0, stream, zt, ds_enc, wtc, wtdc, y_cls, sums);
-    hipLaunchKernelGGL(k_bnfin, dim3(1), dim3(256), 0, stream, sums, bn_cls_g, bn_cls_b, bn_reg_g, bn_reg_b, ss);
-    hipLaunchKernelGGL(k_lin_cls, dim3(64), dim3(256), 0, stream, y_cls, ss, lin_cls_w, out);
-    hipLaunchKernelGGL(k_lin_reg2, dim3(512), dim3(256), 0, stream, y_reg, ss, lin_reg_w, part);
-    hipLaunchKernelGGL(k_lin_red, dim3(80, 4), dim3(256), 0, stream, part, out + 5120);
-}
+    hipLaunchKernelGGL(k_conv, dim3(1088), dim3(256), 0, stream,
+                       xt, dist_t, zt, ds_enc, wtr, wtdr, wtc, wtdc, y_reg, y_cls, sums);
+    hipLaunchKernelGGL(k_lin, dim3(576), dim3(256), 0, stream,
+                       y_reg, y_cls, sums, bn_cls_g, bn_cls_b, bn_reg_g, bn_reg_b,
+                       lin_reg_w, lin_cls_w, part, out);
+    hipLaunchKernelGGL(k_lin_red, dim3(80, 8), dim3(256), 0, stream, part, out + 5120);
+}
```
